# Kernel tuning notes

Measured on AMD Instinct MI355X. Metric: run time of the kernel, lower is better.

The kernel has to match this reference:

```python
import jax, jax.numpy as jnp
import numpy as np

B = 128          # number of trees (batched identical perfect-binary structure)
LEAVES = 1024    # leaves per tree -> N = 2*LEAVES - 1 = 2047 nodes, heap order
D_IN = 512       # input_size
NL = 64          # num_labels


def setup_inputs() -> dict:
    key = jax.random.key(0)
    k1, k2, k3, k4 = jax.random.split(key, 4)
    N = 2 * LEAVES - 1
    hidden = jax.random.normal(k1, (B, N, D_IN), dtype=jnp.float32)
    W = jax.random.normal(k2, (D_IN, NL), dtype=jnp.float32) / np.sqrt(D_IN)
    b = jax.random.normal(k3, (NL,), dtype=jnp.float32) * 0.02
    trans = jax.random.normal(k4, (NL, NL), dtype=jnp.float32) / np.sqrt(NL)
    return {"hidden": hidden, "W": W, "b": b, "trans": trans}


def reference(hidden, W, b, trans):
    # hidden: [B, N, D] with N = 2^depth - 1 nodes in heap (level) order:
    # node i's children are 2i+1, 2i+2; level d occupies [2^d-1, 2^{d+1}-1).
    Bn, N, D = hidden.shape
    L = trans.shape[0]
    depth = int(np.log2(N + 1))  # number of levels

    # emission scores for every node at once (single_h_pred, no dense layer)
    emis = jnp.einsum('bnd,dl->bnl', hidden, W) + b  # [B, N, L]

    # leaves level
    n = 2 ** (depth - 1)
    inside = emis[:, n - 1: n - 1 + n]  # [B, n, L]

    # inside algorithm, bottom-up:
    # inside[p, a] = emis[p, a]
    #             + logsumexp_l(inside_left[l]  + trans[a, l])
    #             + logsumexp_r(inside_right[r] + trans[a, r])
    for d in range(depth - 2, -1, -1):
        n = 2 ** d
        left = inside[:, 0::2]   # [B, n, L]
        right = inside[:, 1::2]  # [B, n, L]
        lt = jax.nn.logsumexp(left[:, :, None, :] + trans[None, None, :, :], axis=-1)
        rt = jax.nn.logsumexp(right[:, :, None, :] + trans[None, None, :, :], axis=-1)
        inside = emis[:, n - 1: n - 1 + n] + lt + rt  # [B, n, L]

    return inside[:, 0]  # root inside scores, [B, L]
```

## Files before the change

### kernel.cpp

```cpp
#include <hip/hip_runtime.h>
#include <math.h>

#define B_      128
#define NNODES  2047
#define NL_     64
#define DIN     512

typedef __attribute__((ext_vector_type(8))) short short8;
typedef __attribute__((ext_vector_type(4))) float v4f;

static __device__ inline unsigned short f2bf(float x) {
    unsigned u = __float_as_uint(x);
    u = (u + 0x7FFFu + ((u >> 16) & 1u)) >> 16;
    return (unsigned short)u;
}

__global__ __launch_bounds__(256) void kprep(const float* __restrict__ W,
                                             const float* __restrict__ trans,
                                             unsigned short* __restrict__ Wt,
                                             float* __restrict__ E) {
    int i = blockIdx.x * 256 + threadIdx.x;
    if (i < NL_ * NL_) E[i] = __expf(trans[i]);
    int k = i >> 6, n = i & 63;
    Wt[n * DIN + k] = f2bf(W[i]);
}

__global__ __launch_bounds__(256) void kgemm(const float* __restrict__ H,
                                             const unsigned short* __restrict__ Wt,
                                             const float* __restrict__ bias,
                                             float* __restrict__ emis) {
    __shared__ unsigned short Al[64 * 72];
    __shared__ unsigned short Wl[64 * 72];
    int t = threadIdx.x;
    int rowBase = blockIdx.x * 64;
    int lane = t & 63;
    int w    = t >> 6;
    int ln   = lane & 15;
    int quad = lane >> 4;

    v4f acc[4];
    #pragma unroll
    for (int i = 0; i < 4; ++i) acc[i] = (v4f){0.f, 0.f, 0.f, 0.f};

    int r   = t >> 2;
    int sub = t & 3;
    const float* hrow = H + (long)(rowBase + r) * DIN + sub * 16;
    const unsigned short* wrow = Wt + r * DIN + sub * 8;

    for (int kc = 0; kc < DIN; kc += 64) {
        __syncthreads();
        #pragma unroll
        for (int i = 0; i < 4; ++i) {
            float4 v = *(const float4*)(hrow + kc + i * 4);
            unsigned long long pk =
                (unsigned long long)f2bf(v.x)
              | ((unsigned long long)f2bf(v.y) << 16)
              | ((unsigned long long)f2bf(v.z) << 32)
              | ((unsigned long long)f2bf(v.w) << 48);
            *(unsigned long long*)&Al[r * 72 + sub * 16 + i * 4] = pk;
        }
        #pragma unroll
        for (int i = 0; i < 2; ++i) {
            uint4 wv = *(const uint4*)(wrow + kc + i * 32);
            *(uint4*)&Wl[r * 72 + sub * 8 + i * 32] = wv;
        }
        __syncthreads();
        const unsigned short* Ab = &Al[(w * 16 + ln) * 72];
        const unsigned short* Wb = &Wl[ln * 72];
        #pragma unroll
        for (int ks = 0; ks < 2; ++ks) {
            short8 af = *(const short8*)(Ab + ks * 32 + quad * 8);
            #pragma unroll
            for (int nt = 0; nt < 4; ++nt) {
                short8 bf = *(const short8*)(Wb + nt * 16 * 72 + ks * 32 + quad * 8);
                acc[nt] = __builtin_amdgcn_mfma_f32_16x16x32_bf16(af, bf, acc[nt], 0, 0, 0);
            }
        }
    }
    #pragma unroll
    for (int nt = 0; nt < 4; ++nt) {
        float bv = bias[nt * 16 + ln];
        #pragma unroll
        for (int rg = 0; rg < 4; ++rg) {
            int row = rowBase + w * 16 + quad * 4 + rg;
            emis[(long)row * NL_ + nt * 16 + ln] = acc[nt][rg] + bv;
        }
    }
}

template<int JW>
__global__ __launch_bounds__(256, 4) void klevel2(float* __restrict__ inside,
                                                  const float* __restrict__ E,
                                                  int d) {
    constexpr int JS = 16 / JW;
    __shared__ float Ls[128 * 64];
    __shared__ float ms[128];
    int t = threadIdx.x;
    int n = 1 << d;
    int gpb = n >> 6;
    int group = blockIdx.x / JS;
    int js    = blockIdx.x - group * JS;
    int b  = group / gpb;
    int i0 = (group - b * gpb) << 6;
    int g0 = n - 1 + i0;
    long cbase = ((long)(b * NNODES + 2 * g0 + 1)) << 6;

    const float4* src = (const float4*)(inside + cbase);
    #pragma unroll
    for (int it = 0; it < 8; ++it) {
        int q   = t + it * 256;
        int row = q >> 4, slot = q & 15;
        float4 v = src[q];
        *(float4*)&Ls[row * 64 + ((slot ^ ((row >> 1) & 15)) << 2)] = v;
    }
    __syncthreads();

    {
        int row  = t >> 1, half = t & 1;
        int pk   = (row >> 1) & 15;
        float vals[32];
        #pragma unroll
        for (int q = 0; q < 8; ++q) {
            int slot = half * 8 + q;
            float4 v = *(const float4*)&Ls[row * 64 + ((slot ^ pk) << 2)];
            vals[4*q] = v.x; vals[4*q+1] = v.y; vals[4*q+2] = v.z; vals[4*q+3] = v.w;
        }
        float m = vals[0];
        #pragma unroll
        for (int k = 1; k < 32; ++k) m = fmaxf(m, vals[k]);
        m = fmaxf(m, __shfl_xor(m, 1));
        #pragma unroll
        for (int k = 0; k < 32; ++k) vals[k] = __expf(vals[k] - m);
        #pragma unroll
        for (int q = 0; q < 8; ++q) {
            int slot = half * 8 + q;
            *(float4*)&Ls[row * 64 + ((slot ^ pk) << 2)] =
                (float4){vals[4*q], vals[4*q+1], vals[4*q+2], vals[4*q+3]};
        }
        if (half == 0) ms[row] = m;
    }
    __syncthreads();

    int p  = t & 63;
    int w  = t >> 6;
    int j0 = (js * 4 + w) * JW;
    float accl[JW], accr[JW];
    #pragma unroll
    for (int j = 0; j < JW; ++j) { accl[j] = 0.f; accr[j] = 0.f; }

    #pragma unroll
    for (int c = 0; c < 4; ++c) {
        float el[16], er[16];
        #pragma unroll
        for (int q = 0; q < 4; ++q) {
            int sl = ((c * 4 + q) ^ (p & 15)) << 2;
            float4 v = *(const float4*)&Ls[(2 * p)     * 64 + sl];
            float4 u = *(const float4*)&Ls[(2 * p + 1) * 64 + sl];
            el[4*q]=v.x; el[4*q+1]=v.y; el[4*q+2]=v.z; el[4*q+3]=v.w;
            er[4*q]=u.x; er[4*q+1]=u.y; er[4*q+2]=u.z; er[4*q+3]=u.w;
        }
        #pragma unroll
        for (int j = 0; j < JW; ++j) {
            const float4* Er = (const float4*)(E + ((j0 + j) << 6) + c * 16);
            #pragma unroll
            for (int q = 0; q < 4; ++q) {
                float4 e = Er[q];
                accl[j] = fmaf(el[4*q+0], e.x, accl[j]);
                accl[j] = fmaf(el[4*q+1], e.y, accl[j]);
                accl[j] = fmaf(el[4*q+2], e.z, accl[j]);
                accl[j] = fmaf(el[4*q+3], e.w, accl[j]);
                accr[j] = fmaf(er[4*q+0], e.x, accr[j]);
                accr[j] = fmaf(er[4*q+1], e.y, accr[j]);
                accr[j] = fmaf(er[4*q+2], e.z, accr[j]);
                accr[j] = fmaf(er[4*q+3], e.w, accr[j]);
            }
        }
    }

    float mbase = ms[2 * p] + ms[2 * p + 1];
    #pragma unroll
    for (int j = 0; j < JW; ++j)
        accl[j] = mbase + __logf(accl[j]) + __logf(accr[j]);

    long prow = ((long)(b * NNODES + g0 + p)) << 6;
    if constexpr (JW >= 4) {
        #pragma unroll
        for (int j4 = 0; j4 < JW; j4 += 4) {
            float4* pg = (float4*)(inside + prow + j0 + j4);
            float4 ev = *pg;
            ev.x += accl[j4]; ev.y += accl[j4+1];
            ev.z += accl[j4+2]; ev.w += accl[j4+3];
            *pg = ev;
        }
    } else {
        float2* pg = (float2*)(inside + prow + j0);
        float2 ev = *pg;
        ev.x += accl[0]; ev.y += accl[1];
        *pg = ev;
    }
}

__global__ __launch_bounds__(256) void ktail(float* __restrict__ inside,
                                             const float* __restrict__ E,
                                             float* __restrict__ out) {
    int b    = blockIdx.x;
    int lane = threadIdx.x & 63;
    int wid  = threadIdx.x >> 6;

    float Ereg[64];
    const float4* E4 = (const float4*)(E + lane * NL_);
    #pragma unroll
    for (int q = 0; q < 16; ++q) {
        float4 v = E4[q];
        Ereg[4*q] = v.x; Ereg[4*q+1] = v.y; Ereg[4*q+2] = v.z; Ereg[4*q+3] = v.w;
    }
    int base = b * NNODES;

    for (int d = 5; d >= 0; --d) {
        int n = 1 << d;
        for (int i = wid; i < n; i += 4) {
            int g    = n - 1 + i;
            int rowC = (base + 2 * g + 1) << 6;
            float lf = inside[rowC + lane];
            float rf = inside[rowC + 64 + lane];
            float ml = lf, mr = rf;
            #pragma unroll
            for (int s = 32; s >= 1; s >>= 1) {
                ml = fmaxf(ml, __shfl_xor(ml, s));
                mr = fmaxf(mr, __shfl_xor(mr, s));
            }
            float el = __expf(lf - ml);
            float er = __expf(rf - mr);
            float accl = 0.f, accr = 0.f;
            #pragma unroll
            for (int k = 0; k < 64; ++k) {
                float ek = __int_as_float(__builtin_amdgcn_readlane(__float_as_int(el), k));
                float rk = __int_as_float(__builtin_amdgcn_readlane(__float_as_int(er), k));
                accl = fmaf(ek, Ereg[k], accl);
                accr = fmaf(rk, Ereg[k], accr);
            }
            int rowG  = (base + g) << 6;
            float res = inside[rowG + lane] + ml + mr + __logf(accl) + __logf(accr);
            if (d == 0) out[b * NL_ + lane] = res;
            else        inside[rowG + lane] = res;
        }
        __syncthreads();
    }
}

extern "C" void kernel_launch(void* const* d_in, const int* in_sizes, int n_in,
                              void* d_out, int out_size, void* d_ws, size_t ws_size,
                              hipStream_t stream) {
    const float* hidden = (const float*)d_in[0];
    const float* W      = (const float*)d_in[1];
    const float* bias   = (const float*)d_in[2];
    const float* trans  = (const float*)d_in[3];
    float* out = (float*)d_out;
    float* E   = (float*)d_ws;
    unsigned short* Wt = (unsigned short*)(E + NL_ * NL_);
    float* inside = E + NL_ * NL_ + (DIN * NL_ / 2);

    kprep<<<(DIN * NL_) / 256, 256, 0, stream>>>(W, trans, Wt, E);
    kgemm<<<(B_ * NNODES) / 64, 256, 0, stream>>>(hidden, Wt, bias, inside);
    klevel2<16><<<((B_ << 9) >> 6) * 1, 256, 0, stream>>>(inside, E, 9);
    klevel2< 8><<<((B_ << 8) >> 6) * 2, 256, 0, stream>>>(inside, E, 8);
    klevel2< 4><<<((B_ << 7) >> 6) * 4, 256, 0, stream>>>(inside, E, 7);
    klevel2< 2><<<((B_ << 6) >> 6) * 8, 256, 0, stream>>>(inside, E, 6);
    ktail<<<B_, 256, 0, stream>>>(inside, E, out);
}
```

Baseline: 812.2 us.

## Double-buffer GEMM tiles with direct global-to-LDS loads and async level loads

The emission GEMM now stages fp32 hidden tiles and bf16 weight tiles straight into shared memory with global_load_lds, double-buffered so the next K chunk loads while MFMAs run on the current one. The fp32-to-bf16 conversion moves from the store path to after the LDS read, with XOR swizzles on the source addresses to avoid bank conflicts. The level kernel's child-row load also switches to global_load_lds with the swizzle moved onto the global address. This doubles the fp32 LDS footprint per block and repeats the bf16 conversion for each K step, which may lower occupancy.

```diff
diff --git a/kernel.cpp b/kernel.cpp
--- a/kernel.cpp
+++ b/kernel.cpp
@@ -9,10 +9,22 @@
 typedef __attribute__((ext_vector_type(8))) short short8;
 typedef __attribute__((ext_vector_type(4))) float v4f;
 
+#define GLL(g, l) __builtin_amdgcn_global_load_lds(                      \
+    (const __attribute__((address_space(1))) void*)(g),                  \
+    (__attribute__((address_space(3))) void*)(l), 16, 0, 0)
+
 static __device__ inline unsigned short f2bf(float x) {
     unsigned u = __float_as_uint(x);
     u = (u + 0x7FFFu + ((u >> 16) & 1u)) >> 16;
     return (unsigned short)u;
+}
+
+static __device__ inline short8 cvt8(float4 u, float4 v) {
+    short8 r;
+    unsigned short* p = (unsigned short*)&r;
+    p[0] = f2bf(u.x); p[1] = f2bf(u.y); p[2] = f2bf(u.z); p[3] = f2bf(u.w);
+    p[4] = f2bf(v.x); p[5] = f2bf(v.y); p[6] = f2bf(v.z); p[7] = f2bf(v.w);
+    return r;
 }
 
 __global__ __launch_bounds__(256) void kprep(const float* __restrict__ W,
@@ -29,61 +41,76 @@
                                              const unsigned short* __restrict__ Wt,
                                              const float* __restrict__ bias,
                                              float* __restrict__ emis) {
-    __shared__ unsigned short Al[64 * 72];
-    __shared__ unsigned short Wl[64 * 72];
-    int t = threadIdx.x;
-    int rowBase = blockIdx.x * 64;
+    __shared__ float Af[2][64 * 64];
+    __shared__ unsigned short Wl[2][64 * 64];
+    int t    = threadIdx.x;
     int lane = t & 63;
     int w    = t >> 6;
     int ln   = lane & 15;
     int quad = lane >> 4;
+    long rowBase = (long)blockIdx.x * 64;
+
+    const float* asrc[4];
+    #pragma unroll
+    for (int i = 0; i < 4; ++i) {
+        int q = i * 256 + t, row = q >> 4, s = q & 15;
+        asrc[i] = H + (rowBase + row) * DIN + ((s ^ (row & 15)) << 2);
+    }
+    const unsigned short* wsrc[2];
+    #pragma unroll
+    for (int i = 0; i < 2; ++i) {
+        int q = i * 256 + t, row = q >> 3, s = q & 7;
+        wsrc[i] = Wt + row * DIN + ((s ^ (row & 7)) << 3);
+    }
+    int woff = w * 1024;
 
     v4f acc[4];
     #pragma unroll
     for (int i = 0; i < 4; ++i) acc[i] = (v4f){0.f, 0.f, 0.f, 0.f};
 
-    int r   = t >> 2;
-    int sub = t & 3;
-    const float* hrow = H + (long)(rowBase + r) * DIN + sub * 16;
-    const unsigned short* wrow = Wt + r * DIN + sub * 8;
-
+    #pragma unroll
+    for (int i = 0; i < 4; ++i) GLL(asrc[i], (char*)&Af[0][0] + i * 4096 + woff);
+    #pragma unroll
+    for (int i = 0; i < 2; ++i) GLL(wsrc[i], (char*)&Wl[0][0] + i * 4096 + woff);
+    __syncthreads();
+
+    int cur = 0;
+    #pragma unroll
     for (int kc = 0; kc < DIN; kc += 64) {
+        if (kc + 64 < DIN) {
+            #pragma unroll
+            for (int i = 0; i < 4; ++i)
+                GLL(asrc[i] + kc + 64, (char*)&Af[cur ^ 1][0] + i * 4096 + woff);
+            #pragma unroll
+            for (int i = 0; i < 2; ++i)
+                GLL(wsrc[i] + kc + 64, (char*)&Wl[cur ^ 1][0] + i * 4096 + woff);
+        }
+        const char* Ab = (const char*)&Af[cur][0] + (w * 16 + ln) * 256;
+        const char* Wb = (const char*)&Wl[cur][0];
+        #pragma unroll
+        for (int ks = 0; ks < 2; ++ks) {
+            int s0 = ks * 8 + quad * 2;
+            float4 alo = *(const float4*)(Ab + ((s0 ^ ln) << 4));
+            float4 ahi = *(const float4*)(Ab + (((s0 + 1) ^ ln) << 4));
+            short8 af = cvt8(alo, ahi);
+            #pragma unroll
+            for (int nt = 0; nt < 4; ++nt) {
+                const char* Wr = Wb + (nt * 16 + ln) * 128;
+                short8 bf = *(const short8*)(Wr + (((ks * 4 + quad) ^ (ln & 7)) << 4));
+                acc[nt] = __builtin_amdgcn_mfma_f32_16x16x32_bf16(af, bf, acc[nt], 0, 0, 0);
+            }
+        }
         __syncthreads();
-        #pragma unroll
-        for (int i = 0; i < 4; ++i) {
-            float4 v = *(const float4*)(hrow + kc + i * 4);
-            unsigned long long pk =
-                (unsigned long long)f2bf(v.x)
-              | ((unsigned long long)f2bf(v.y) << 16)
-              | ((unsigned long long)f2bf(v.z) << 32)
-              | ((unsigned long long)f2bf(v.w) << 48);
-            *(unsigned long long*)&Al[r * 72 + sub * 16 + i * 4] = pk;
-        }
-        #pragma unroll
-        for (int i = 0; i < 2; ++i) {
-            uint4 wv = *(const uint4*)(wrow + kc + i * 32);
-            *(uint4*)&Wl[r * 72 + sub * 8 + i * 32] = wv;
-        }
-        __syncthreads();
-        const unsigned short* Ab = &Al[(w * 16 + ln) * 72];
-        const unsigned short* Wb = &Wl[ln * 72];
-        #pragma unroll
-        for (int ks = 0; ks < 2; ++ks) {
-            short8 af = *(const short8*)(Ab + ks * 32 + quad * 8);
-            #pragma unroll
-            for (int nt = 0; nt < 4; ++nt) {
-                short8 bf = *(const short8*)(Wb + nt * 16 * 72 + ks * 32 + quad * 8);
-                acc[nt] = __builtin_amdgcn_mfma_f32_16x16x32_bf16(af, bf, acc[nt], 0, 0, 0);
-            }
-        }
-    }
+        cur ^= 1;
+    }
+
     #pragma unroll
     for (int nt = 0; nt < 4; ++nt) {
         float bv = bias[nt * 16 + ln];
         #pragma unroll
         for (int rg = 0; rg < 4; ++rg) {
-            int row = rowBase + w * 16 + quad * 4 + rg;
-            emis[(long)row * NL_ + nt * 16 + ln] = acc[nt][rg] + bv;
+            long row = rowBase + w * 16 + quad * 4 + rg;
+            emis[row * NL_ + nt * 16 + ln] = acc[nt][rg] + bv;
         }
     }
 }
@@ -105,13 +132,14 @@
     int g0 = n - 1 + i0;
     long cbase = ((long)(b * NNODES + 2 * g0 + 1)) << 6;
 
-    const float4* src = (const float4*)(inside + cbase);
+    const float* srcf = inside + cbase;
+    int wv = t >> 6;
     #pragma unroll
     for (int it = 0; it < 8; ++it) {
-        int q   = t + it * 256;
-        int row = q >> 4, slot = q & 15;
-        float4 v = src[q];
-        *(float4*)&Ls[row * 64 + ((slot ^ ((row >> 1) & 15)) << 2)] = v;
+        int q = it * 256 + t;
+        int row = q >> 4, s = q & 15;
+        GLL(srcf + row * 64 + ((s ^ ((row >> 1) & 15)) << 2),
+            (char*)Ls + it * 4096 + wv * 1024);
     }
     __syncthreads();
 
```

Result: no change. 811.0 us (-0.2%).
